# Kernel tuning notes

Measured on AMD Instinct MI355X. Metric: run time of the kernel, lower is better.

Reference implementation:

```python
import jax, jax.numpy as jnp
import numpy as np

H, W = 512, 512
G = 8192
ALPHA_THRESH = 1.0 / 255.0        # meta_f32[0]
TRANS_THRESH = 1.0e-4             # meta_f32[1]
ALPHA_CAP = 0.99                  # meta_f32[6]
BG = jnp.zeros((3,), dtype=jnp.float32)  # config.background


def setup_inputs() -> dict:
    key = jax.random.key(0)
    ks = jax.random.split(key, 7)
    mx = jax.random.uniform(ks[0], (G,), minval=0.0, maxval=float(W))
    my = jax.random.uniform(ks[1], (G,), minval=0.0, maxval=float(H))
    means2d = jnp.stack([mx, my], axis=-1)
    # Build valid conics (inverse 2x2 covariances) from random rotation + scales
    theta = jax.random.uniform(ks[2], (G,), minval=0.0, maxval=2.0 * np.pi)
    s = jax.random.uniform(ks[3], (G, 2), minval=2.0, maxval=12.0)  # px stddevs
    ct, st = jnp.cos(theta), jnp.sin(theta)
    v1, v2 = s[:, 0] ** 2, s[:, 1] ** 2
    ca = ct * ct * v1 + st * st * v2
    cb = ct * st * (v1 - v2)
    cc = st * st * v1 + ct * ct * v2
    det = ca * cc - cb * cb
    conics = jnp.stack([cc / det, -cb / det, ca / det], axis=-1)  # [G,3] = (a,b,c)
    colors = jax.random.uniform(ks[4], (G, 3))
    opacities = jax.random.uniform(ks[5], (G,))
    depths = jax.random.uniform(ks[6], (G,), minval=0.1, maxval=100.0)
    return {"means2d": means2d, "conics": conics, "colors": colors,
            "opacities": opacities, "depths": depths}


def reference(means2d, conics, colors, opacities, depths):
    # Stable front-to-back depth sort (mirrors perm = argsort(depths, stable))
    perm = jnp.argsort(depths, stable=True)
    m = means2d[perm]
    cn = conics[perm]
    col = colors[perm]
    op = opacities[perm]
    a, b, c = cn[:, 0], cn[:, 1], cn[:, 2]
    px = jnp.arange(W, dtype=means2d.dtype) + 0.5  # pixel centers

    def row(y):
        py = y.astype(means2d.dtype) + 0.5
        dx = px[:, None] - m[None, :, 0]          # [W,G]
        dy = py - m[:, 1]                          # [G]
        sigma = 0.5 * (a * dx * dx + c * dy * dy) + b * dx * dy  # [W,G]
        alpha = jnp.minimum(ALPHA_CAP, op * jnp.exp(-sigma))
        alpha = jnp.where((sigma < 0) | (alpha < ALPHA_THRESH), 0.0, alpha)
        # exclusive cumulative transmittance along depth order
        Tprev = jnp.cumprod(1.0 - alpha, axis=-1)
        Tprev = jnp.concatenate([jnp.ones((W, 1), alpha.dtype), Tprev[:, :-1]], axis=-1)
        # early-termination: splats seen after T drops below threshold contribute 0
        wgt = alpha * Tprev * (Tprev >= TRANS_THRESH)  # [W,G]
        rgb = wgt @ col                                 # [W,3]
        t_rem = 1.0 - wgt.sum(axis=-1)                  # remaining transmittance
        return rgb + t_rem[:, None] * BG

    return jax.lax.map(row, jnp.arange(H))  # [H,W,3]
```

## Files before the change

### kernel.cpp

```cpp
#include <hip/hip_runtime.h>
#include <hip/hip_fp16.h>

#define G 8192
#define IMG_W 512
#define IMG_H 512
#define TILE 16
#define NTX (IMG_W / TILE)
#define NTY (IMG_H / TILE)
#define BLK 256
#define BLK2 128
#define CAP 1024
#define ALPHA_THRESH (1.0f/255.0f)
#define ALPHA_CAP 0.99f
#define TRANS_THRESH 1e-4f

__global__ __launch_bounds__(BLK)
void range_kernel(const float* __restrict__ means2d,
                  const float* __restrict__ conics,
                  const float* __restrict__ opac,
                  unsigned int* __restrict__ ranges)
{
    int g = blockIdx.x * BLK + threadIdx.x;
    if (g >= G) return;
    float op = opac[g];
    unsigned int packed = 0xFFu;
    if (op * 255.0f >= 1.0f) {
        float smax = __logf(op * 255.0f);
        float a = conics[3*g], b = conics[3*g+1], c = conics[3*g+2];
        float det = fmaxf(a * c - b * b, 1e-12f);
        float rx = sqrtf(fmaxf(2.0f * smax * c / det, 0.0f)) * 1.0001f + 0.01f;
        float ry = sqrtf(fmaxf(2.0f * smax * a / det, 0.0f)) * 1.0001f + 0.01f;
        float mx = means2d[2*g], my = means2d[2*g+1];
        int txmin = (int)ceilf ((mx - rx - 15.5f) * 0.0625f);
        int txmax = (int)floorf((mx + rx -  0.5f) * 0.0625f);
        int tymin = (int)ceilf ((my - ry - 15.5f) * 0.0625f);
        int tymax = (int)floorf((my + ry -  0.5f) * 0.0625f);
        if (!(txmax < 0 || txmin > NTX-1 || tymax < 0 || tymin > NTY-1 ||
              txmin > txmax || tymin > tymax)) {
            txmin = max(txmin, 0); txmax = min(txmax, NTX-1);
            tymin = max(tymin, 0); tymax = min(tymax, NTY-1);
            packed = (unsigned)txmin | ((unsigned)txmax << 8)
                   | ((unsigned)tymin << 16) | ((unsigned)tymax << 24);
        }
    }
    ranges[g] = packed;
}

__device__ __forceinline__ int hitp(unsigned p, unsigned btx, unsigned bty)
{
    return (btx >= (p & 0xffu)) & (btx <= ((p >> 8) & 0xffu)) &
           (bty >= ((p >> 16) & 0xffu)) & (bty <= (p >> 24));
}

__global__ __launch_bounds__(BLK2)
void tile_kernel(const unsigned int* __restrict__ ranges,
                 const float* __restrict__ depths,
                 const float* __restrict__ means2d,
                 const float* __restrict__ conics,
                 const float* __restrict__ colors,
                 const float* __restrict__ opac,
                 float*       __restrict__ out)
{
    __shared__ unsigned short slist[CAP];
    __shared__ unsigned long long keys[CAP];
    __shared__ int woff[2];
    __shared__ float4 buf[BLK2 * 2];

    const int t = threadIdx.x;
    const int lane = t & 63, w = t >> 6;
    const unsigned btx = blockIdx.x, bty = blockIdx.y;

    const uint4* r4 = (const uint4*)ranges;
    const int wq = w * (4096 / 4);

    int cnt = 0;
    #pragma unroll 4
    for (int i = 0; i < 16; ++i) {
        uint4 rv = r4[wq + i * 64 + lane];
        cnt += hitp(rv.x, btx, bty) + hitp(rv.y, btx, bty)
             + hitp(rv.z, btx, bty) + hitp(rv.w, btx, bty);
    }
    #pragma unroll
    for (int d = 1; d < 64; d <<= 1) cnt += __shfl_xor(cnt, d);
    if (lane == 0) woff[w] = cnt;
    __syncthreads();

    int offs = (w == 1) ? woff[0] : 0;
    const int N = min(woff[0] + woff[1], CAP);

    const unsigned long long lt = (1ull << lane) - 1ull;
    #pragma unroll 4
    for (int i = 0; i < 16; ++i) {
        uint4 rv = r4[wq + i * 64 + lane];
        int gbase = w * 4096 + i * 256 + lane * 4;
        int h0 = hitp(rv.x, btx, bty), h1 = hitp(rv.y, btx, bty);
        int h2 = hitp(rv.z, btx, bty), h3 = hitp(rv.w, btx, bty);
        unsigned long long m0 = __ballot(h0), m1 = __ballot(h1);
        unsigned long long m2 = __ballot(h2), m3 = __ballot(h3);
        int pos = offs + __popcll(m0 & lt) + __popcll(m1 & lt)
                       + __popcll(m2 & lt) + __popcll(m3 & lt);
        if (h0) { if (pos < CAP) slist[pos] = (unsigned short)(gbase    ); pos++; }
        if (h1) { if (pos < CAP) slist[pos] = (unsigned short)(gbase + 1); pos++; }
        if (h2) { if (pos < CAP) slist[pos] = (unsigned short)(gbase + 2); pos++; }
        if (h3) { if (pos < CAP) slist[pos] = (unsigned short)(gbase + 3); pos++; }
        offs += __popcll(m0) + __popcll(m1) + __popcll(m2) + __popcll(m3);
    }
    __syncthreads();

    for (int i = t; i < N; i += BLK2) {
        unsigned idx = slist[i];
        keys[i] = ((unsigned long long)__float_as_uint(depths[idx]) << 13)
                | (unsigned long long)idx;
    }
    __syncthreads();
    for (int i = t; i < N; i += BLK2) {
        unsigned long long ke = keys[i];
        int r = 0;
        #pragma unroll 4
        for (int j = 0; j < N; ++j) r += (keys[j] < ke);
        slist[r] = (unsigned short)(ke & 0x1fffull);
    }
    __syncthreads();

    const int x  = btx * TILE + (lane & 15);
    const int y0 = bty * TILE + w * 4 + (lane >> 4);
    const float px  = (float)x  + 0.5f;
    const float py0 = (float)y0 + 0.5f;
    const float py1 = py0 + 8.0f;

    float T0 = 1.f, T1 = 1.f;
    float r0a = 0.f, g0a = 0.f, b0a = 0.f;
    float r1a = 0.f, g1a = 0.f, b1a = 0.f;
    bool done = false;

    for (int base = 0; base < N; base += BLK2) {
        const int n = min(BLK2, N - base);
        float4 q0 = make_float4(0.f, 0.f, 0.f, 0.f);
        float4 q1 = make_float4(0.f, 0.f, 0.f, 0.f);
        if (t < n) {
            int idx = slist[base + t];
            union { float f; __half2 h; } uc;
            uc.h = __floats2half2_rn(colors[3*idx], colors[3*idx + 1]);
            q0 = make_float4(means2d[2*idx], means2d[2*idx + 1],
                             0.5f * conics[3*idx], conics[3*idx + 1]);
            q1 = make_float4(0.5f * conics[3*idx + 2], opac[idx],
                             uc.f, colors[3*idx + 2]);
        }
        buf[t * 2] = q0; buf[t * 2 + 1] = q1;
        __syncthreads();

        if (!done) {
            const int n8 = (n + 7) & ~7;
            for (int j = 0; j < n8 && !done; j += 8) {
                #pragma unroll
                for (int u = 0; u < 8; ++u) {
                    float4 c0 = buf[(j + u) * 2];
                    float4 c1 = buf[(j + u) * 2 + 1];
                    float dx  = px - c0.x;
                    float bdx = c0.w * dx;
                    float txx = c0.z * dx * dx;
                    float dy0 = py0 - c0.y;
                    float dy1 = py1 - c0.y;
                    float s0  = fmaf(fmaf(c1.x, dy0, bdx), dy0, txx);
                    float s1  = fmaf(fmaf(c1.x, dy1, bdx), dy1, txx);
                    union { float f; __half2 h; } uc; uc.f = c1.z;
                    float cr = __low2float(uc.h);
                    float cg = __high2float(uc.h);
                    float cb = c1.w;
                    float e0 = c1.y * __expf(-s0);
                    float e1 = c1.y * __expf(-s1);
                    float a0 = (s0 >= 0.f && e0 >= ALPHA_THRESH)
                             ? fminf(e0, ALPHA_CAP) : 0.f;
                    float a1 = (s1 >= 0.f && e1 >= ALPHA_THRESH)
                             ? fminf(e1, ALPHA_CAP) : 0.f;
                    float w0 = a0 * T0, w1 = a1 * T1;
                    r0a = fmaf(w0, cr, r0a); g0a = fmaf(w0, cg, g0a);
                    b0a = fmaf(w0, cb, b0a);
                    r1a = fmaf(w1, cr, r1a); g1a = fmaf(w1, cg, g1a);
                    b1a = fmaf(w1, cb, b1a);
                    T0 *= (1.f - a0); T1 *= (1.f - a1);
                }
                if (!__any(fmaxf(T0, T1) >= TRANS_THRESH)) done = true;
            }
        }
        if (__syncthreads_and((int)done)) break;
    }

    int o = (y0 * IMG_W + x) * 3;
    out[o] = r0a; out[o + 1] = g0a; out[o + 2] = b0a;
    o = ((y0 + 8) * IMG_W + x) * 3;
    out[o] = r1a; out[o + 1] = g1a; out[o + 2] = b1a;
}

extern "C" void kernel_launch(void* const* d_in, const int* in_sizes, int n_in,
                              void* d_out, int out_size, void* d_ws, size_t ws_size,
                              hipStream_t stream)
{
    const float* means2d = (const float*)d_in[0];
    const float* conics  = (const float*)d_in[1];
    const float* colors  = (const float*)d_in[2];
    const float* opac    = (const float*)d_in[3];
    const float* depths  = (const float*)d_in[4];
    float* out = (float*)d_out;
    unsigned int* ranges = (unsigned int*)d_ws;

    range_kernel<<<G / BLK, BLK, 0, stream>>>(means2d, conics, opac, ranges);
    tile_kernel<<<dim3(NTX, NTY), BLK2, 0, stream>>>(
        ranges, depths, means2d, conics, colors, opac, out);
}
```

Measured before the change: 94.29 us.

## Use 16x8 tiles with single-wave blocks and fuse key build into compaction

Result: slower. 102.5 us (+8.7%).

```diff
diff --git a/kernel.cpp b/kernel.cpp
--- a/kernel.cpp
+++ b/kernel.cpp
@@ -6,9 +6,8 @@
 #define IMG_H 512
 #define TILE 16
 #define NTX (IMG_W / TILE)
-#define NTY (IMG_H / TILE)
+#define NTY8 (IMG_H / 8)
 #define BLK 256
-#define BLK2 128
 #define CAP 1024
 #define ALPHA_THRESH (1.0f/255.0f)
 #define ALPHA_CAP 0.99f
@@ -33,12 +32,12 @@
         float mx = means2d[2*g], my = means2d[2*g+1];
         int txmin = (int)ceilf ((mx - rx - 15.5f) * 0.0625f);
         int txmax = (int)floorf((mx + rx -  0.5f) * 0.0625f);
-        int tymin = (int)ceilf ((my - ry - 15.5f) * 0.0625f);
-        int tymax = (int)floorf((my + ry -  0.5f) * 0.0625f);
-        if (!(txmax < 0 || txmin > NTX-1 || tymax < 0 || tymin > NTY-1 ||
+        int tymin = (int)ceilf ((my - ry -  7.5f) * 0.125f);
+        int tymax = (int)floorf((my + ry -  0.5f) * 0.125f);
+        if (!(txmax < 0 || txmin > NTX-1 || tymax < 0 || tymin > NTY8-1 ||
               txmin > txmax || tymin > tymax)) {
             txmin = max(txmin, 0); txmax = min(txmax, NTX-1);
-            tymin = max(tymin, 0); tymax = min(tymax, NTY-1);
+            tymin = max(tymin, 0); tymax = min(tymax, NTY8-1);
             packed = (unsigned)txmin | ((unsigned)txmax << 8)
                    | ((unsigned)tymin << 16) | ((unsigned)tymax << 24);
         }
@@ -52,7 +51,7 @@
            (bty >= ((p >> 16) & 0xffu)) & (bty <= (p >> 24));
 }
 
-__global__ __launch_bounds__(BLK2)
+__global__ __launch_bounds__(64)
 void tile_kernel(const unsigned int* __restrict__ ranges,
                  const float* __restrict__ depths,
                  const float* __restrict__ means2d,
@@ -61,59 +60,50 @@
                  const float* __restrict__ opac,
                  float*       __restrict__ out)
 {
+    __shared__ unsigned long long keys[CAP];
     __shared__ unsigned short slist[CAP];
-    __shared__ unsigned long long keys[CAP];
-    __shared__ int woff[2];
-    __shared__ float4 buf[BLK2 * 2];
+    __shared__ float4 buf[128];
 
-    const int t = threadIdx.x;
-    const int lane = t & 63, w = t >> 6;
+    const int lane = threadIdx.x;
     const unsigned btx = blockIdx.x, bty = blockIdx.y;
 
     const uint4* r4 = (const uint4*)ranges;
-    const int wq = w * (4096 / 4);
-
-    int cnt = 0;
-    #pragma unroll 4
-    for (int i = 0; i < 16; ++i) {
-        uint4 rv = r4[wq + i * 64 + lane];
-        cnt += hitp(rv.x, btx, bty) + hitp(rv.y, btx, bty)
-             + hitp(rv.z, btx, bty) + hitp(rv.w, btx, bty);
-    }
-    #pragma unroll
-    for (int d = 1; d < 64; d <<= 1) cnt += __shfl_xor(cnt, d);
-    if (lane == 0) woff[w] = cnt;
-    __syncthreads();
-
-    int offs = (w == 1) ? woff[0] : 0;
-    const int N = min(woff[0] + woff[1], CAP);
-
     const unsigned long long lt = (1ull << lane) - 1ull;
-    #pragma unroll 4
-    for (int i = 0; i < 16; ++i) {
-        uint4 rv = r4[wq + i * 64 + lane];
-        int gbase = w * 4096 + i * 256 + lane * 4;
+    int pos = 0;
+    for (int i = 0; i < 32; ++i) {
+        uint4 rv = r4[i * 64 + lane];
+        int gbase = i * 256 + lane * 4;
         int h0 = hitp(rv.x, btx, bty), h1 = hitp(rv.y, btx, bty);
         int h2 = hitp(rv.z, btx, bty), h3 = hitp(rv.w, btx, bty);
         unsigned long long m0 = __ballot(h0), m1 = __ballot(h1);
         unsigned long long m2 = __ballot(h2), m3 = __ballot(h3);
-        int pos = offs + __popcll(m0 & lt) + __popcll(m1 & lt)
-                       + __popcll(m2 & lt) + __popcll(m3 & lt);
-        if (h0) { if (pos < CAP) slist[pos] = (unsigned short)(gbase    ); pos++; }
-        if (h1) { if (pos < CAP) slist[pos] = (unsigned short)(gbase + 1); pos++; }
-        if (h2) { if (pos < CAP) slist[pos] = (unsigned short)(gbase + 2); pos++; }
-        if (h3) { if (pos < CAP) slist[pos] = (unsigned short)(gbase + 3); pos++; }
-        offs += __popcll(m0) + __popcll(m1) + __popcll(m2) + __popcll(m3);
+        int p = pos + __popcll(m0 & lt) + __popcll(m1 & lt)
+                    + __popcll(m2 & lt) + __popcll(m3 & lt);
+        if (h0 && p < CAP) {
+            keys[p] = ((unsigned long long)__float_as_uint(depths[gbase]) << 13)
+                    | (unsigned)gbase;
+        }
+        p += h0;
+        if (h1 && p < CAP) {
+            keys[p] = ((unsigned long long)__float_as_uint(depths[gbase+1]) << 13)
+                    | (unsigned)(gbase + 1);
+        }
+        p += h1;
+        if (h2 && p < CAP) {
+            keys[p] = ((unsigned long long)__float_as_uint(depths[gbase+2]) << 13)
+                    | (unsigned)(gbase + 2);
+        }
+        p += h2;
+        if (h3 && p < CAP) {
+            keys[p] = ((unsigned long long)__float_as_uint(depths[gbase+3]) << 13)
+                    | (unsigned)(gbase + 3);
+        }
+        pos += __popcll(m0) + __popcll(m1) + __popcll(m2) + __popcll(m3);
     }
+    const int N = min(pos, CAP);
     __syncthreads();
 
-    for (int i = t; i < N; i += BLK2) {
-        unsigned idx = slist[i];
-        keys[i] = ((unsigned long long)__float_as_uint(depths[idx]) << 13)
-                | (unsigned long long)idx;
-    }
-    __syncthreads();
-    for (int i = t; i < N; i += BLK2) {
+    for (int i = lane; i < N; i += 64) {
         unsigned long long ke = keys[i];
         int r = 0;
         #pragma unroll 4
@@ -123,22 +113,22 @@
     __syncthreads();
 
     const int x  = btx * TILE + (lane & 15);
-    const int y0 = bty * TILE + w * 4 + (lane >> 4);
+    const int y0 = bty * 8 + (lane >> 4);
     const float px  = (float)x  + 0.5f;
     const float py0 = (float)y0 + 0.5f;
-    const float py1 = py0 + 8.0f;
+    const float py1 = py0 + 4.0f;
 
     float T0 = 1.f, T1 = 1.f;
     float r0a = 0.f, g0a = 0.f, b0a = 0.f;
     float r1a = 0.f, g1a = 0.f, b1a = 0.f;
     bool done = false;
 
-    for (int base = 0; base < N; base += BLK2) {
-        const int n = min(BLK2, N - base);
+    for (int base = 0; base < N && !done; base += 64) {
+        const int n = min(64, N - base);
         float4 q0 = make_float4(0.f, 0.f, 0.f, 0.f);
         float4 q1 = make_float4(0.f, 0.f, 0.f, 0.f);
-        if (t < n) {
-            int idx = slist[base + t];
+        if (lane < n) {
+            int idx = slist[base + lane];
             union { float f; __half2 h; } uc;
             uc.h = __floats2half2_rn(colors[3*idx], colors[3*idx + 1]);
             q0 = make_float4(means2d[2*idx], means2d[2*idx + 1],
@@ -146,49 +136,47 @@
             q1 = make_float4(0.5f * conics[3*idx + 2], opac[idx],
                              uc.f, colors[3*idx + 2]);
         }
-        buf[t * 2] = q0; buf[t * 2 + 1] = q1;
+        buf[lane * 2] = q0; buf[lane * 2 + 1] = q1;
         __syncthreads();
 
-        if (!done) {
-            const int n8 = (n + 7) & ~7;
-            for (int j = 0; j < n8 && !done; j += 8) {
-                #pragma unroll
-                for (int u = 0; u < 8; ++u) {
-                    float4 c0 = buf[(j + u) * 2];
-                    float4 c1 = buf[(j + u) * 2 + 1];
-                    float dx  = px - c0.x;
-                    float bdx = c0.w * dx;
-                    float txx = c0.z * dx * dx;
-                    float dy0 = py0 - c0.y;
-                    float dy1 = py1 - c0.y;
-                    float s0  = fmaf(fmaf(c1.x, dy0, bdx), dy0, txx);
-                    float s1  = fmaf(fmaf(c1.x, dy1, bdx), dy1, txx);
-                    union { float f; __half2 h; } uc; uc.f = c1.z;
-                    float cr = __low2float(uc.h);
-                    float cg = __high2float(uc.h);
-                    float cb = c1.w;
-                    float e0 = c1.y * __expf(-s0);
-                    float e1 = c1.y * __expf(-s1);
-                    float a0 = (s0 >= 0.f && e0 >= ALPHA_THRESH)
-                             ? fminf(e0, ALPHA_CAP) : 0.f;
-                    float a1 = (s1 >= 0.f && e1 >= ALPHA_THRESH)
-                             ? fminf(e1, ALPHA_CAP) : 0.f;
-                    float w0 = a0 * T0, w1 = a1 * T1;
-                    r0a = fmaf(w0, cr, r0a); g0a = fmaf(w0, cg, g0a);
-                    b0a = fmaf(w0, cb, b0a);
-                    r1a = fmaf(w1, cr, r1a); g1a = fmaf(w1, cg, g1a);
-                    b1a = fmaf(w1, cb, b1a);
-                    T0 *= (1.f - a0); T1 *= (1.f - a1);
-                }
-                if (!__any(fmaxf(T0, T1) >= TRANS_THRESH)) done = true;
+        const int n8 = (n + 7) & ~7;
+        for (int j = 0; j < n8 && !done; j += 8) {
+            #pragma unroll
+            for (int u = 0; u < 8; ++u) {
+                float4 c0 = buf[(j + u) * 2];
+                float4 c1 = buf[(j + u) * 2 + 1];
+                float dx  = px - c0.x;
+                float bdx = c0.w * dx;
+                float txx = c0.z * dx * dx;
+                float dy0 = py0 - c0.y;
+                float dy1 = py1 - c0.y;
+                float s0  = fmaf(fmaf(c1.x, dy0, bdx), dy0, txx);
+                float s1  = fmaf(fmaf(c1.x, dy1, bdx), dy1, txx);
+                union { float f; __half2 h; } uc; uc.f = c1.z;
+                float cr = __low2float(uc.h);
+                float cg = __high2float(uc.h);
+                float cb = c1.w;
+                float e0 = c1.y * __expf(-s0);
+                float e1 = c1.y * __expf(-s1);
+                float a0 = (s0 >= 0.f && e0 >= ALPHA_THRESH)
+                         ? fminf(e0, ALPHA_CAP) : 0.f;
+                float a1 = (s1 >= 0.f && e1 >= ALPHA_THRESH)
+                         ? fminf(e1, ALPHA_CAP) : 0.f;
+                float w0 = a0 * T0, w1 = a1 * T1;
+                r0a = fmaf(w0, cr, r0a); g0a = fmaf(w0, cg, g0a);
+                b0a = fmaf(w0, cb, b0a);
+                r1a = fmaf(w1, cr, r1a); g1a = fmaf(w1, cg, g1a);
+                b1a = fmaf(w1, cb, b1a);
+                T0 *= (1.f - a0); T1 *= (1.f - a1);
             }
+            if (!__any(fmaxf(T0, T1) >= TRANS_THRESH)) done = true;
         }
-        if (__syncthreads_and((int)done)) break;
+        __syncthreads();
     }
 
     int o = (y0 * IMG_W + x) * 3;
     out[o] = r0a; out[o + 1] = g0a; out[o + 2] = b0a;
-    o = ((y0 + 8) * IMG_W + x) * 3;
+    o = ((y0 + 4) * IMG_W + x) * 3;
     out[o] = r1a; out[o + 1] = g1a; out[o + 2] = b1a;
 }
 
@@ -205,6 +193,6 @@
     unsigned int* ranges = (unsigned int*)d_ws;
 
     range_kernel<<<G / BLK, BLK, 0, stream>>>(means2d, conics, opac, ranges);
-    tile_kernel<<<dim3(NTX, NTY), BLK2, 0, stream>>>(
+    tile_kernel<<<dim3(NTX, NTY8), 64, 0, stream>>>(
         ranges, depths, means2d, conics, colors, opac, out);
 }
```
